# Optimization experiments

Measured on AMD Instinct MI355X. Metric: run time of the kernel, lower is better.

The kernel has to match this reference:

```python
import jax, jax.numpy as jnp
import numpy as np

BS, S, N, C, H, CP, T, CT, NB = 1, 2, 2048, 128, 8, 16, 512, 384, 3
DH = C // H
INF = 1.0e8

def _ln(x, w, b, eps=1e-5):
    mu = jnp.mean(x, axis=-1, keepdims=True)
    var = jnp.var(x, axis=-1, keepdims=True)
    return (x - mu) * jax.lax.rsqrt(var + eps) * w + b

def _ln_na(x, eps=1e-5):
    mu = jnp.mean(x, axis=-1, keepdims=True)
    var = jnp.var(x, axis=-1, keepdims=True)
    return (x - mu) * jax.lax.rsqrt(var + eps)

def _betas(n):
    # query row l belongs to window centered at 32*(l//32)+16; keys within +/- n_keys//2=64
    l = jnp.arange(n)
    centers = (l // 32) * 32 + 16
    m = jnp.arange(n)
    ok = (m[None, :] >= (centers - 64)[:, None]) & (m[None, :] < (centers + 64)[:, None])
    return jnp.where(ok, 0.0, -INF).astype(jnp.float32)

def setup_inputs():
    key = jax.random.key(0)
    ks = iter(jax.random.split(key, 80))
    def W(*shape):
        return jax.random.normal(next(ks), shape, dtype=jnp.float32) * 0.05
    return {
        "atom_single": jax.random.normal(next(ks), (BS, S, N, C), dtype=jnp.float32),
        "atom_proj": jax.random.normal(next(ks), (BS, N, C), dtype=jnp.float32),
        "atom_pair": jax.random.normal(next(ks), (BS, N, N, CP), dtype=jnp.float32),
        "mask": jnp.ones((BS, N), jnp.float32),
        "tok_idx": jnp.sort(jax.random.randint(next(ks), (BS, N), 0, T), axis=-1),
        "aln_s_w": jnp.ones((NB, C), jnp.float32), "aln_s_b": jnp.zeros((NB, C), jnp.float32),
        "aln_gate_w": W(NB, C, C), "aln_gate_b": jnp.zeros((NB, C), jnp.float32),
        "aln_shift_w": W(NB, C, C),
        "q_w": W(NB, C, C), "q_b": jnp.zeros((NB, C), jnp.float32),
        "k_w": W(NB, C, C), "v_w": W(NB, C, C),
        "pair_ln_w": jnp.ones((NB, CP), jnp.float32), "pair_ln_b": jnp.zeros((NB, CP), jnp.float32),
        "pair_w": W(NB, CP, H),
        "gate_w": W(NB, C, C), "out_w": W(NB, C, C),
        "og_w": W(NB, C, C), "og_b": jnp.full((NB, C), -2.0, jnp.float32),
        "t_aln_s_w": jnp.ones((NB, C), jnp.float32), "t_aln_s_b": jnp.zeros((NB, C), jnp.float32),
        "t_aln_gate_w": W(NB, C, C), "t_aln_gate_b": jnp.zeros((NB, C), jnp.float32),
        "t_aln_shift_w": W(NB, C, C),
        "t_a_w": W(NB, C, 2 * C), "t_b_w": W(NB, C, 2 * C),
        "t_out_w": W(NB, 2 * C, C),
        "t_og_w": W(NB, C, C), "t_og_b": jnp.full((NB, C), -2.0, jnp.float32),
        "tok_w": W(C, CT),
    }

def _forward(atom_single, atom_proj, atom_pair, mask, tok_idx, aln_s_w, aln_s_b, aln_gate_w, aln_gate_b, aln_shift_w, q_w, q_b, k_w, v_w, pair_ln_w, pair_ln_b, pair_w, gate_w, out_w, og_w, og_b, t_aln_s_w, t_aln_s_b, t_aln_gate_w, t_aln_gate_b, t_aln_shift_w, t_a_w, t_b_w, t_out_w, t_og_w, t_og_b, tok_w):
    betas = _betas(N)[None, None, None]                        # [1,1,1,N,N]
    mask_bias = ((mask - 1.0) * INF)[:, None, None, None, :]   # [bs,1,1,1,N]
    s = atom_proj[:, None]                                     # [bs,1,N,C]
    a = atom_single                                            # [bs,S,N,C]
    for i in range(NB):
        # AttentionPairBias with AdaLN conditioning on s
        sn = _ln(s, aln_s_w[i], aln_s_b[i])
        a1 = jax.nn.sigmoid(sn @ aln_gate_w[i] + aln_gate_b[i]) * _ln_na(a) + sn @ aln_shift_w[i]
        q = (a1 @ q_w[i] + q_b[i]).reshape(BS, S, N, H, DH)
        k = (a1 @ k_w[i]).reshape(BS, S, N, H, DH)
        v = (a1 @ v_w[i]).reshape(BS, S, N, H, DH)
        zb = _ln(atom_pair, pair_ln_w[i], pair_ln_b[i]) @ pair_w[i]    # [bs,N,N,H]
        zb = jnp.transpose(zb, (0, 3, 1, 2))[:, None]                  # [bs,1,H,N,N]
        logits = jnp.einsum('bsqhd,bskhd->bshqk', q, k) / np.float32(np.sqrt(DH)) + zb + betas + mask_bias
        p = jax.nn.softmax(logits, axis=-1)
        o = jnp.einsum('bshqk,bskhd->bsqhd', p, v).reshape(BS, S, N, C)
        o = (jax.nn.sigmoid(a1 @ gate_w[i]) * o) @ out_w[i]
        a = a + jax.nn.sigmoid(sn @ og_w[i] + og_b[i]) * o
        # ConditionedTransitionBlock (SwiGLU with adaLN-Zero gating)
        sn2 = _ln(s, t_aln_s_w[i], t_aln_s_b[i])
        a2 = jax.nn.sigmoid(sn2 @ t_aln_gate_w[i] + t_aln_gate_b[i]) * _ln_na(a) + sn2 @ t_aln_shift_w[i]
        hidden = jax.nn.silu(a2 @ t_a_w[i]) * (a2 @ t_b_w[i])
        a = a + jax.nn.sigmoid(sn2 @ t_og_w[i] + t_og_b[i]) * (hidden @ t_out_w[i])
    # project to token dim, relu, scatter-mean atoms -> tokens
    q_tok = jax.nn.relu(a @ tok_w)                             # [bs,S,N,CT]
    oh = jax.nn.one_hot(tok_idx, T, dtype=q_tok.dtype)         # [bs,N,T]
    cnt = jnp.clip(jnp.sum(oh, axis=1), 1.0)                   # [bs,T]
    tok = jnp.einsum('bsnc,bnt->bstc', q_tok, oh) / cnt[:, None, :, None]
    return tok

def reference(atom_single, atom_proj, atom_pair, mask, tok_idx, aln_s_w, aln_s_b, aln_gate_w, aln_gate_b, aln_shift_w, q_w, q_b, k_w, v_w, pair_ln_w, pair_ln_b, pair_w, gate_w, out_w, og_w, og_b, t_aln_s_w, t_aln_s_b, t_aln_gate_w, t_aln_gate_b, t_aln_shift_w, t_a_w, t_b_w, t_out_w, t_og_w, t_og_b, tok_w):
    return _forward(atom_single, atom_proj, atom_pair, mask, tok_idx, aln_s_w, aln_s_b, aln_gate_w, aln_gate_b, aln_shift_w, q_w, q_b, k_w, v_w, pair_ln_w, pair_ln_b, pair_w, gate_w, out_w, og_w, og_b, t_aln_s_w, t_aln_s_b, t_aln_gate_w, t_aln_gate_b, t_aln_shift_w, t_a_w, t_b_w, t_out_w, t_og_w, t_og_b, tok_w)
```

## Files before the change

### kernel.cpp

```cpp
#include <hip/hip_runtime.h>
#include <math.h>

#define NATOM 2048
#define CD 128
#define SD 2
#define TT 512
#define CTD 384
#define NBI 3
#define MR 4096

typedef unsigned short ushortx;
typedef __attribute__((ext_vector_type(8))) short bf16x8;
typedef __attribute__((ext_vector_type(4))) float f32x4;
typedef __attribute__((ext_vector_type(4))) unsigned short us4;

__device__ __forceinline__ float sigm(float x){ return 1.0f/(1.0f+expf(-x)); }
__device__ __forceinline__ ushortx f2b(float f){
  union { float f; unsigned u; } v; v.f = f;
  unsigned r = v.u + 0x7fffu + ((v.u>>16)&1u);
  return (ushortx)(r>>16);
}
__device__ __forceinline__ float b2f(ushortx u){
  union { unsigned u; float f; } v; v.u = ((unsigned)u)<<16; return v.f;
}
union U8 { ushortx u[8]; float4 v; };

#define OFFB_W3T    0ll
#define OFFB_B3     589824ll
#define OFFB_WQKVGT 599040ll
#define OFFB_BQ     992256ll
#define OFFB_WOUTT  998400ll
#define OFFB_WABT   1096704ll
#define OFFB_WTOUTT 1489920ll
#define OFFB_WTOKT  1686528ll
#define OFFB_SNP    2833408ll
#define OFFB_A      12270592ll
#define OFFB_QKVG   14367744ll
#define OFFB_ZB     18562048ll
#define OFFB_QTOK   31144960ll
#define OFFB_QKVG2  37436416ll

struct WPtrs {
  const float *aln_gate_w, *aln_gate_b, *aln_shift_w, *og_w, *og_b;
  const float *t_aln_gate_w, *t_aln_gate_b, *t_aln_shift_w, *t_og_w, *t_og_b;
  const float *q_w, *q_b, *k_w, *v_w, *gate_w, *out_w;
  const float *t_a_w, *t_b_w, *t_out_w, *tok_w;
};

__global__ __launch_bounds__(256) void prologue_kernel(WPtrs P, char* __restrict__ wsb,
  const float* __restrict__ atom_pair,
  const float* __restrict__ plw, const float* __restrict__ plb, const float* __restrict__ pw)
{
  int b = blockIdx.x;
  if (b < 3471){
    long long idx = (long long)b*256 + threadIdx.x;
    const long long s0=294912, s1=2304, s2=196608, s3=1536, s4=49152, s5=196608, s6=98304;
    if (idx < s0) {
      int which = (int)(idx/49152); int r = (int)(idx%49152); int n=r/128, k=r%128;
      int i = which>>1, t = which&1;
      const float* src;
      if (n<128)      src = (t?P.t_aln_gate_w :P.aln_gate_w ) + i*16384 + k*128 + n;
      else if (n<256) src = (t?P.t_aln_shift_w:P.aln_shift_w) + i*16384 + k*128 + (n-128);
      else            src = (t?P.t_og_w       :P.og_w       ) + i*16384 + k*128 + (n-256);
      ((ushortx*)(wsb+OFFB_W3T))[idx] = f2b(*src); return;
    }
    idx -= s0;
    if (idx < s1) {
      int which = (int)(idx/384); int col = (int)(idx%384); int i=which>>1, t=which&1;
      float v = 0.f;
      if (col<128)       v = (t?P.t_aln_gate_b:P.aln_gate_b)[i*128+col];
      else if (col>=256) v = (t?P.t_og_b      :P.og_b      )[i*128+col-256];
      ((float*)(wsb+OFFB_B3))[idx] = v; return;
    }
    idx -= s1;
    if (idx < s2) {
      int i = (int)(idx/65536); int r = (int)(idx%65536); int n=r/128, k=r%128;
      int seg = n>>7, c = n&127;
      const float* src = (seg==0?P.q_w: seg==1?P.k_w: seg==2?P.v_w: P.gate_w) + i*16384 + k*128 + c;
      ((ushortx*)(wsb+OFFB_WQKVGT))[idx] = f2b(*src); return;
    }
    idx -= s2;
    if (idx < s3) {
      int i = (int)(idx/512); int col = (int)(idx%512);
      ((float*)(wsb+OFFB_BQ))[idx] = (col<128) ? P.q_b[i*128+col] : 0.f; return;
    }
    idx -= s3;
    if (idx < s4) {
      int i = (int)(idx/16384); int r = (int)(idx%16384); int n=r/128, k=r%128;
      ((ushortx*)(wsb+OFFB_WOUTT))[idx] = f2b(P.out_w[i*16384 + k*128 + n]); return;
    }
    idx -= s4;
    if (idx < s5) {
      int i = (int)(idx/65536); int r = (int)(idx%65536); int n=r/128, k=r%128;
      const float* src = (n<256) ? P.t_a_w + i*32768 + k*256 + n
                                 : P.t_b_w + i*32768 + k*256 + (n-256);
      ((ushortx*)(wsb+OFFB_WABT))[idx] = f2b(*src); return;
    }
    idx -= s5;
    if (idx < s6) {
      int i = (int)(idx/32768); int r = (int)(idx%32768); int n=r/256, k=r%256;
      ((ushortx*)(wsb+OFFB_WTOUTT))[idx] = f2b(P.t_out_w[i*32768 + k*128 + n]); return;
    }
    idx -= s6;
    {
      int n = (int)(idx/128); int k = (int)(idx%128);
      ((ushortx*)(wsb+OFFB_WTOKT))[idx] = f2b(P.tok_w[k*384 + n]); return;
    }
  }
  {
    int idx = (b-3471)*256 + threadIdx.x;
    int q = idx>>7, j = idx&127;
    int m = (q & ~31) - 48 + j;
    bool ok = (m>=0 && m<NATOM);
    float x[16]; float mu=0.f, rs=0.f;
    if (ok){
      float s=0.f, sq=0.f;
      const float* p = atom_pair + ((long long)q*NATOM + m)*16;
      #pragma unroll
      for (int c=0;c<16;c++){ x[c]=p[c]; s+=x[c]; sq+=x[c]*x[c]; }
      mu = s*(1.f/16.f); float var = sq*(1.f/16.f)-mu*mu; rs = rsqrtf(var+1e-5f);
    }
    ushortx* zb = (ushortx*)(wsb+OFFB_ZB);
    #pragma unroll
    for (int it=0; it<NBI; it++){
      float out[8] = {0,0,0,0,0,0,0,0};
      if (ok){
        #pragma unroll
        for (int c=0;c<16;c++){
          float xn = (x[c]-mu)*rs*plw[it*16+c] + plb[it*16+c];
          #pragma unroll
          for (int h=0;h<8;h++) out[h] += xn * pw[it*128 + c*8 + h];
        }
      }
      #pragma unroll
      for (int h=0;h<8;h++)
        zb[(((long long)it*8+h)*NATOM + q)*128 + j] = f2b(out[h]);
    }
  }
}

template<int LAST>
__global__ __launch_bounds__(256) void fused_iter(
  const float* __restrict__ Afsrc,
  float* __restrict__ Af,
  const ushortx* __restrict__ QKVGin,
  const ushortx* __restrict__ zb,
  const float* __restrict__ mask,
  const ushortx* __restrict__ Wout,
  const ushortx* __restrict__ Wab,
  const ushortx* __restrict__ Wtout,
  const ushortx* __restrict__ WN,
  const float*   __restrict__ biasN,
  const ushortx* __restrict__ snpA,
  const ushortx* __restrict__ snpT,
  const ushortx* __restrict__ snpN,
  ushortx* __restrict__ QKVGout,
  float*   __restrict__ QTOK)
{
  __shared__ __align__(16) ushortx Bt[2][64][136];
  __shared__ __align__(16) float   Afr[16][132];
  __shared__ __align__(16) ushortx A2t[16][136];
  __shared__ __align__(16) ushortx Ht[16][264];
  __shared__ __align__(16) ushortx XX[16*264];
  __shared__ __align__(16) ushortx Kh[2][128][24];
  __shared__ __align__(16) ushortx Vh[2][128][24];
  __shared__ __align__(16) ushortx Zh[2][16][136];
  __shared__ __align__(16) ushortx Qh[2][16][16];
  __shared__ __align__(16) ushortx Gh[2][16][16];
  __shared__ __align__(16) float   Ls[16][132];
  __shared__ __align__(16) ushortx SnpT[16][392];
  __shared__ __align__(16) ushortx SnpN[16][392];
  __shared__ __align__(16) ushortx SnpAog[16][136];
  __shared__ float maskb[128];
  ushortx (*A1t)[136] = (ushortx(*)[136])XX;
  ushortx (*Hs)[264]  = (ushortx(*)[264])XX;

  int tid = threadIdx.x, rowBase = blockIdx.x*16;
  int sIdx = rowBase >> 11;
  int n0 = rowBase & 2047;
  int wbase = (n0 & ~31) - 48;
  int wave=tid>>6, lane=tid&63, lr=lane&15, lk=(lane>>4)*8;
  int wc = wave*16;
  int r = tid>>4, tcol = tid&15, c8 = tcol*8;
  long long grow = rowBase + r;
  int sr=tid>>2, csB=(tid&3)*32;
  int crow = (lane>>4)*4;

  { const float4* ap=(const float4*)&Afsrc[grow*128+c8];
    *(float4*)&Afr[r][c8]=ap[0]; *(float4*)&Afr[r][c8+4]=ap[1]; }
  if (tid < 128){
    int m = wbase + tid;
    maskb[tid] = (m>=0 && m<NATOM) ? (mask[m]-1.0f)*1e8f : -1e30f;
  }
  #pragma unroll
  for (int k=0;k<3;k++){ int idx=tid+k*256; int rr=idx/48, cc=(idx%48)*8;
    *(float4*)&SnpT[rr][cc] = *(const float4*)&snpT[(long long)((rowBase+rr)&2047)*384 + cc]; }
  if (!LAST){
    #pragma unroll
    for (int k=0;k<3;k++){ int idx=tid+k*256; int rr=idx/48, cc=(idx%48)*8;
      *(float4*)&SnpN[rr][cc] = *(const float4*)&snpN[(long long)((rowBase+rr)&2047)*384 + cc]; }
  }
  *(float4*)&SnpAog[r][c8] = *(const float4*)&snpA[(long long)((rowBase+r)&2047)*384 + 256 + c8];
  {
    const float4* bg = (const float4*)(Wout + (long long)sr*128 + csB);
    #pragma unroll
    for (int u=0;u<4;u++) *(float4*)&Bt[0][sr][csB+u*8] = bg[u];
  }

  int jr=tid>>1, hf=tid&1;
  int mm=wbase+jr; int mc = mm<0?0:(mm>NATOM-1?NATOM-1:mm);
  long long krow = ((long long)(sIdx*NATOM+mc))*512;
  auto issue = [&](int h, float4&kreg, float4&vreg, float4&zreg, float4&qg){
    kreg = *(const float4*)&QKVGin[krow + 128 + h*16 + hf*8];
    vreg = *(const float4*)&QKVGin[krow + 256 + h*16 + hf*8];
    zreg = *(const float4*)&zb[((long long)h*NATOM + n0 + r)*128 + c8];
    if (tid < 32)
      qg = *(const float4*)&QKVGin[((long long)(rowBase+(tid>>1)))*512 + h*16 + (tid&1)*8];
    else if (tid < 64){
      int tt=tid-32;
      qg = *(const float4*)&QKVGin[((long long)(rowBase+(tt>>1)))*512 + 384 + h*16 + (tt&1)*8];
    }
  };
  auto commit = [&](int bb, float4 kreg, float4 vreg, float4 zreg, float4 qg){
    *(float4*)&Kh[bb][jr][hf*8] = kreg;
    *(float4*)&Vh[bb][jr][hf*8] = vreg;
    *(float4*)&Zh[bb][r][c8] = zreg;
    if (tid < 32) *(float4*)&Qh[bb][tid>>1][(tid&1)*8] = qg;
    else if (tid < 64){ int tt=tid-32; *(float4*)&Gh[bb][tt>>1][(tt&1)*8] = qg; }
  };
  { float4 k0,v0,z0,q0 = make_float4(0,0,0,0);
    issue(0,k0,v0,z0,q0); commit(0,k0,v0,z0,q0); }
  __syncthreads();
  for (int h=0; h<8; ++h){
    int bb=h&1;
    float4 kn,vn,zn,qn = make_float4(0,0,0,0);
    if (h<7) issue(h+1,kn,vn,zn,qn);
    float qv[16];
    { U8 qa,qb_;
      qa.v=*(const float4*)&Qh[bb][r][0]; qb_.v=*(const float4*)&Qh[bb][r][8];
      #pragma unroll
      for (int t=0;t<8;t++){ qv[t]=b2f(qa.u[t]); qv[8+t]=b2f(qb_.u[t]); } }
    float lv[8], pmax=-1e30f;
    #pragma unroll
    for (int u=0;u<8;u++){
      int j=tcol+u*16;
      U8 ka,kb_;
      ka.v=*(const float4*)&Kh[bb][j][0]; kb_.v=*(const float4*)&Kh[bb][j][8];
      float dot=0.f;
      #pragma unroll
      for (int t=0;t<8;t++) dot += qv[t]*b2f(ka.u[t]);
      #pragma unroll
      for (int t=0;t<8;t++) dot += qv[8+t]*b2f(kb_.u[t]);
      float L = dot*0.25f + b2f(Zh[bb][r][j]) + maskb[j];
      lv[u]=L; pmax=fmaxf(pmax,L);
    }
    #pragma unroll
    for (int off=1; off<16; off<<=1) pmax = fmaxf(pmax, __shfl_xor(pmax,off));
    float ps=0.f;
    #pragma unroll
    for (int u=0;u<8;u++){ float e=expf(lv[u]-pmax); Ls[r][tcol+u*16]=e; ps+=e; }
    #pragma unroll
    for (int off=1; off<16; off<<=1) ps += __shfl_xor(ps,off);
    float inv = 1.0f/ps;
    __syncthreads();
    float a0=0.f;
    #pragma unroll 4
    for (int j=0;j<128;j++) a0 += Ls[r][j]*b2f(Vh[bb][j][tcol]);
    float gt = b2f(Gh[bb][r][tcol]);
    A1t[r][h*16+tcol] = f2b(sigm(gt)*a0*inv);
    if (h<7) commit((h+1)&1,kn,vn,zn,qn);
    __syncthreads();
  }

  const int NP = LAST ? 20 : 22;
  f32x4 acc = (f32x4){0.f,0.f,0.f,0.f};
  for (int p=0; p<NP; p++){
    __syncthreads();
    if (p+1 < NP){
      int pn = p+1;
      const ushortx* bsrc; long long bstride;
      if (pn<2)      { bsrc = Wout  + (long long)(pn*64)*128;                      bstride=128; }
      else if (pn<10){ bsrc = Wab   + (long long)((pn-2)*64)*128;                  bstride=128; }
      else if (pn<14){ int q=pn-10; bsrc = Wtout + (long long)((q>>1)*64)*256 + (q&1)*128; bstride=256; }
      else           { int q=pn-14; bsrc = WN    + (long long)(q*64)*128;          bstride=128; }
      const float4* bg=(const float4*)(bsrc + (long long)sr*bstride + csB);
      #pragma unroll
      for (int u=0;u<4;u++) *(float4*)&Bt[pn&1][sr][csB+u*8] = bg[u];
    }
    if (p==2){
      float x[8], s=0.f, sq=0.f;
      #pragma unroll
      for (int u=0;u<8;u++){ x[u]=Afr[r][c8+u]; s+=x[u]; sq+=x[u]*x[u]; }
      #pragma unroll
      for (int off=1; off<16; off<<=1){ s+=__shfl_xor(s,off); sq+=__shfl_xor(sq,off); }
      float mu=s*(1.f/128.f), rs=rsqrtf(sq*(1.f/128.f)-mu*mu+1e-5f);
      U8 ga,ha,pk;
      ga.v=*(const float4*)&SnpT[r][c8]; ha.v=*(const float4*)&SnpT[r][128+c8];
      #pragma unroll
      for (int t=0;t<8;t++) pk.u[t]=f2b(sigm(b2f(ga.u[t]))*((x[t]-mu)*rs)+b2f(ha.u[t]));
      *(float4*)&A2t[r][c8]=pk.v;
      __syncthreads();
    }
    if (p==14){
      float x[8], s=0.f, sq=0.f;
      #pragma unroll
      for (int u=0;u<8;u++){ x[u]=Afr[r][c8+u]; s+=x[u]; sq+=x[u]*x[u]; }
      { float4* ap=(float4*)&Af[grow*128+c8];
        ap[0]=*(float4*)&Afr[r][c8]; ap[1]=*(float4*)&Afr[r][c8+4]; }
      if (LAST){
        U8 pk;
        #pragma unroll
        for (int t=0;t<8;t++) pk.u[t]=f2b(x[t]);
        *(float4*)&A2t[r][c8]=pk.v;
      } else {
        #pragma unroll
        for (int off=1; off<16; off<<=1){ s+=__shfl_xor(s,off); sq+=__shfl_xor(sq,off); }
        float mu=s*(1.f/128.f), rs=rsqrtf(sq*(1.f/128.f)-mu*mu+1e-5f);
        U8 ga,ha,pk;
        ga.v=*(const float4*)&SnpN[r][c8]; ha.v=*(const float4*)&SnpN[r][128+c8];
        #pragma unroll
        for (int t=0;t<8;t++) pk.u[t]=f2b(sigm(b2f(ga.u[t]))*((x[t]-mu)*rs)+b2f(ha.u[t]));
        *(float4*)&A2t[r][c8]=pk.v;
      }
      __syncthreads();
    }
    if (p!=11 && p!=13) acc=(f32x4){0.f,0.f,0.f,0.f};
    #pragma unroll
    for (int ks=0; ks<4; ks++){
      bf16x8 a;
      if (p<2)       a = *(const bf16x8*)&A1t[lr][ks*32+lk];
      else if (p<10) a = *(const bf16x8*)&A2t[lr][ks*32+lk];
      else if (p<14){ int kc=(p-10)&1; a = *(const bf16x8*)&Hs[lr][kc*128+ks*32+lk]; }
      else           a = *(const bf16x8*)&A2t[lr][ks*32+lk];
      bf16x8 b = *(const bf16x8*)&Bt[p&1][wc+lr][ks*32+lk];
      acc = __builtin_amdgcn_mfma_f32_16x16x32_bf16(a,b,acc,0,0,0);
    }
    if (p<2){
      int ccol = p*64 + wc + lr;
      #pragma unroll
      for (int rr=0;rr<4;rr++){
        int rrow=crow+rr;
        float g=b2f(SnpAog[rrow][ccol]);
        Afr[rrow][ccol]+=sigm(g)*acc[rr];
      }
    } else if (p<10){
      int cp=p-2; int ccol=cp*64+wc+lr;
      if (cp<4){
        #pragma unroll
        for (int rr=0;rr<4;rr++) Ht[crow+rr][ccol]=f2b(acc[rr]);
      } else {
        int hc=ccol-256;
        #pragma unroll
        for (int rr=0;rr<4;rr++){
          float ha=b2f(Ht[crow+rr][hc]);
          Hs[crow+rr][hc]=f2b(ha*sigm(ha)*acc[rr]);
        }
      }
    } else if (p==11 || p==13){
      int cp=(p-10)>>1; int ccol=cp*64+wc+lr;
      #pragma unroll
      for (int rr=0;rr<4;rr++){
        int rrow=crow+rr;
        float g=b2f(SnpT[rrow][256+ccol]);
        Afr[rrow][ccol]+=sigm(g)*acc[rr];
      }
    } else if (p>=14){
      int q=p-14; int ccol=q*64+wc+lr;
      if (LAST){
        #pragma unroll
        for (int rr=0;rr<4;rr++)
          QTOK[(long long)(rowBase+crow+rr)*384 + ccol]=fmaxf(acc[rr],0.f);
      } else {
        float bv=biasN[ccol];
        #pragma unroll
        for (int rr=0;rr<4;rr++)
          QKVGout[(long long)(rowBase+crow+rr)*512 + ccol]=f2b(acc[rr]+bv);
      }
    }
  }
}

template<int AM, int BM>
__global__ __launch_bounds__(256) void gemm_f(
    const void* __restrict__ Asrc, long long strideA,
    const ushortx* __restrict__ B, long long strideB,
    const float* __restrict__ bias, long long strideBias,
    void* Cv, long long strideC,
    int M, int N, int K, int mode,
    const void* __restrict__ p1, const void* __restrict__ p2,
    const void* __restrict__ p3, const void* __restrict__ p4)
{
  constexpr int CG  = 256/BM;
  constexpr int XC  = 128/CG;
  constexpr int F4  = XC/8;
  constexpr int ACI = BM/32;
  int z = blockIdx.z;
  B += z*strideB;
  if (bias) bias += z*strideBias;
  float* C = (float*)Cv + z*strideC;
  ushortx* Cu = (ushortx*)Cv + z*strideC;
  __shared__ __align__(16) ushortx At[BM][136];
  __shared__ __align__(16) ushortx Bt[64][136];
  int tid = threadIdx.x;
  int rowBase = blockIdx.y*BM, colBase = blockIdx.x*64;
  int wave = tid>>6, lane = tid&63;
  int wr = (wave>>1)*(BM/2), wc = (wave&1)*32;
  int lr = lane&15, lk = (lane>>4)*8;
  f32x4 acc[ACI][2];
  #pragma unroll
  for (int i=0;i<ACI;i++)
    #pragma unroll
    for (int j=0;j<2;j++) acc[i][j] = (f32x4){0.f,0.f,0.f,0.f};

  int sr = tid/CG, q = tid%CG, cs = q*XC;
  int row = rowBase + sr;
  int bsr = tid>>2, bq = tid&3, bcs = bq*32;

  for (int kc=0; kc<K; kc+=128){
    if (kc) __syncthreads();
    {
      const float* arow = (const float*)Asrc + (long long)row*128;
      float x[XC]; float s=0.f, sq=0.f;
      const float4* ar = (const float4*)(arow + cs);
      #pragma unroll
      for (int u=0;u<XC/4;u++){
        float4 t = ar[u];
        x[4*u]=t.x; x[4*u+1]=t.y; x[4*u+2]=t.z; x[4*u+3]=t.w;
        s += t.x+t.y+t.z+t.w;
        sq += t.x*t.x+t.y*t.y+t.z*t.z+t.w*t.w;
      }
      #pragma unroll
      for (int off=1; off<CG; off<<=1){ s += __shfl_xor(s,off); sq += __shfl_xor(sq,off); }
      float mu = s*(1.f/128.f), var = sq*(1.f/128.f)-mu*mu;
      float rs = rsqrtf(var + 1e-5f);
      if (AM==1){
        const ushortx* sp = (const ushortx*)p1 + (long long)(row & (NATOM-1))*384;
        const float4* gr = (const float4*)(sp + cs);
        const float4* hr = (const float4*)(sp + 128 + cs);
        #pragma unroll
        for (int u=0;u<F4;u++){
          U8 ga, ha, pk;
          ga.v = gr[u]; ha.v = hr[u];
          #pragma unroll
          for (int t=0;t<8;t++)
            pk.u[t] = f2b(sigm(b2f(ga.u[t]))*((x[8*u+t]-mu)*rs) + b2f(ha.u[t]));
          *(float4*)&At[sr][cs+u*8] = pk.v;
        }
      } else {
        int iw = z>>1, tw = z&1;
        const float* w = (const float*)(tw?p3:p1) + iw*128;
        const float* b = (const float*)(tw?p4:p2) + iw*128;
        const float4* wrp = (const float4*)(w + cs);
        const float4* brp = (const float4*)(b + cs);
        #pragma unroll
        for (int u=0;u<F4;u++){
          float4 wa = wrp[2*u], wb = wrp[2*u+1];
          float4 ba = brp[2*u], bb = brp[2*u+1];
          U8 pk;
          pk.u[0]=f2b((x[8*u  ]-mu)*rs*wa.x+ba.x);
          pk.u[1]=f2b((x[8*u+1]-mu)*rs*wa.y+ba.y);
          pk.u[2]=f2b((x[8*u+2]-mu)*rs*wa.z+ba.z);
          pk.u[3]=f2b((x[8*u+3]-mu)*rs*wa.w+ba.w);
          pk.u[4]=f2b((x[8*u+4]-mu)*rs*wb.x+bb.x);
          pk.u[5]=f2b((x[8*u+5]-mu)*rs*wb.y+bb.y);
          pk.u[6]=f2b((x[8*u+6]-mu)*rs*wb.z+bb.z);
          pk.u[7]=f2b((x[8*u+7]-mu)*rs*wb.w+bb.w);
          *(float4*)&At[sr][cs+u*8] = pk.v;
        }
      }
    }
    {
      const float4* bg = (const float4*)(B + (long long)(colBase+bsr)*K + kc + bcs);
      #pragma unroll
      for (int u=0;u<4;u++) *(float4*)&Bt[bsr][bcs+u*8] = bg[u];
    }
    __syncthreads();
    #pragma unroll
    for (int ks=0; ks<4; ks++){
      bf16x8 b0 = *(const bf16x8*)&Bt[wc+lr][ks*32+lk];
      bf16x8 b1 = *(const bf16x8*)&Bt[wc+16+lr][ks*32+lk];
      #pragma unroll
      for (int i=0;i<ACI;i++){
        bf16x8 a = *(const bf16x8*)&At[wr+i*16+lr][ks*32+lk];
        acc[i][0] = __builtin_amdgcn_mfma_f32_16x16x32_bf16(a,b0,acc[i][0],0,0,0);
        acc[i][1] = __builtin_amdgcn_mfma_f32_16x16x32_bf16(a,b1,acc[i][1],0,0,0);
      }
    }
  }
  int crow0 = rowBase + wr + (lane>>4)*4;
  int ccol0 = colBase + wc + lr;
  #pragma unroll
  for (int i=0;i<ACI;i++){
    #pragma unroll
    for (int j=0;j<2;j++){
      int col = ccol0 + j*16;
      float bv = bias ? bias[col] : 0.f;
      #pragma unroll
      for (int rr=0; rr<4; rr++){
        int rrow = crow0 + i*16 + rr;
        float v = acc[i][j][rr] + bv;
        long long ci = (long long)rrow*N + col;
        Cu[ci] = f2b(v);
        (void)C; (void)mode;
      }
    }
  }
}

__global__ __launch_bounds__(128) void tokagg_kernel(const int* __restrict__ tok_idx,
    const float* __restrict__ qtok, float* __restrict__ out)
{
  int t = blockIdx.x;
  int lo=0, hi=NATOM;
  while (lo<hi){ int mid=(lo+hi)>>1; if (tok_idx[mid] < t) lo=mid+1; else hi=mid; }
  int start = lo;
  lo = start; hi = NATOM;
  while (lo<hi){ int mid=(lo+hi)>>1; if (tok_idx[mid] <= t) lo=mid+1; else hi=mid; }
  int end = lo;
  int cnt = end - start;
  float inv = 1.0f / (float)(cnt>0 ? cnt : 1);
  for (int s=0; s<SD; s++)
    for (int c=threadIdx.x; c<CTD; c+=128){
      float acc = 0.f;
      for (int n=start; n<end; n++) acc += qtok[((long long)(s*NATOM+n))*CTD + c];
      out[(long long)(s*TT + t)*CTD + c] = acc*inv;
    }
}

extern "C" void kernel_launch(void* const* d_in, const int* in_sizes, int n_in,
                              void* d_out, int out_size, void* d_ws, size_t ws_size,
                              hipStream_t stream)
{
  const float* atom_single = (const float*)d_in[0];
  const float* atom_proj   = (const float*)d_in[1];
  const float* atom_pair   = (const float*)d_in[2];
  const float* mask        = (const float*)d_in[3];
  const int*   tok_idx     = (const int*)  d_in[4];
  const float* aln_s_w     = (const float*)d_in[5];
  const float* aln_s_b     = (const float*)d_in[6];
  const float* pair_ln_w   = (const float*)d_in[14];
  const float* pair_ln_b   = (const float*)d_in[15];
  const float* pair_w      = (const float*)d_in[16];
  const float* t_aln_s_w   = (const float*)d_in[21];
  const float* t_aln_s_b   = (const float*)d_in[22];

  char* wsb = (char*)d_ws;
  ushortx* W3T    = (ushortx*)(wsb+OFFB_W3T);
  float*   B3     = (float*)  (wsb+OFFB_B3);
  ushortx* WQKVGT = (ushortx*)(wsb+OFFB_WQKVGT);
  float*   BQ     = (float*)  (wsb+OFFB_BQ);
  ushortx* WOUTT  = (ushortx*)(wsb+OFFB_WOUTT);
  ushortx* WABT   = (ushortx*)(wsb+OFFB_WABT);
  ushortx* WTOUTT = (ushortx*)(wsb+OFFB_WTOUTT);
  ushortx* WTOKT  = (ushortx*)(wsb+OFFB_WTOKT);
  ushortx* SNP    = (ushortx*)(wsb+OFFB_SNP);
  float*   Af     = (float*)  (wsb+OFFB_A);
  ushortx* QKVG   = (ushortx*)(wsb+OFFB_QKVG);
  ushortx* QKVG2  = (ushortx*)(wsb+OFFB_QKVG2);
  ushortx* ZB     = (ushortx*)(wsb+OFFB_ZB);
  float*   QTOK   = (float*)  (wsb+OFFB_QTOK);

  WPtrs P;
  P.aln_gate_w=(const float*)d_in[7];  P.aln_gate_b=(const float*)d_in[8];  P.aln_shift_w=(const float*)d_in[9];
  P.og_w=(const float*)d_in[19]; P.og_b=(const float*)d_in[20];
  P.t_aln_gate_w=(const float*)d_in[23]; P.t_aln_gate_b=(const float*)d_in[24]; P.t_aln_shift_w=(const float*)d_in[25];
  P.t_og_w=(const float*)d_in[29]; P.t_og_b=(const float*)d_in[30];
  P.q_w=(const float*)d_in[10]; P.q_b=(const float*)d_in[11]; P.k_w=(const float*)d_in[12];
  P.v_w=(const float*)d_in[13]; P.gate_w=(const float*)d_in[17]; P.out_w=(const float*)d_in[18];
  P.t_a_w=(const float*)d_in[26]; P.t_b_w=(const float*)d_in[27]; P.t_out_w=(const float*)d_in[28];
  P.tok_w=(const float*)d_in[31];

  prologue_kernel<<<4495,256,0,stream>>>(P, wsb, atom_pair,
      pair_ln_w, pair_ln_b, pair_w);
  gemm_f<4,64><<<dim3(6,32,6),256,0,stream>>>(atom_proj, 0, W3T, 49152ll,
      B3, 384ll, SNP, 786432ll, NATOM, 384, 128, 3,
      aln_s_w, aln_s_b, t_aln_s_w, t_aln_s_b);
  gemm_f<1,64><<<dim3(8,64,1),256,0,stream>>>(atom_single, 0, WQKVGT, 0,
      BQ, 0, QKVG, 0, MR, 512, 128, 3,
      SNP, nullptr, nullptr, nullptr);

  for (int i=0;i<NBI;i++){
    const ushortx* snpA = SNP + (long long)(2*i)*786432;
    const ushortx* snpT = SNP + (long long)(2*i+1)*786432;
    ushortx* qin  = (i&1) ? QKVG2 : QKVG;
    ushortx* qout = (i&1) ? QKVG  : QKVG2;
    const float* afsrc = (i==0) ? atom_single : Af;
    if (i < NBI-1){
      fused_iter<0><<<256,256,0,stream>>>(afsrc, Af, qin,
          ZB + (long long)i*2097152, mask,
          WOUTT + (long long)i*16384, WABT + (long long)i*65536, WTOUTT + (long long)i*32768,
          WQKVGT + (long long)(i+1)*65536, BQ + (long long)(i+1)*512,
          snpA, snpT, SNP + (long long)(2*(i+1))*786432,
          qout, nullptr);
    } else {
      fused_iter<1><<<256,256,0,stream>>>(afsrc, Af, qin,
          ZB + (long long)i*2097152, mask,
          WOUTT + (long long)i*16384, WABT + (long long)i*65536, WTOUTT + (long long)i*32768,
          WTOKT, nullptr,
          snpA, snpT, nullptr,
          qout, QTOK);
    }
  }
  tokagg_kernel<<<TT,128,0,stream>>>(tok_idx, QTOK, (float*)d_out);
}
```

Before: 579.6 us.

## Stage all-head K/V in LDS and fuse token scatter-mean into last iteration

The attention phase now loads the full K and V window (all heads, with an XOR swizzle on K) plus the pair bias into shared memory with one sync, instead of double-buffering each head over eight sync rounds. Heads are processed four at a time with staged probabilities. The separate token-aggregation kernel is removed: the last iteration atomically adds ReLU outputs pre-scaled by per-token inverse counts into an output zeroed in the prologue. Several small shared-memory staging buffers now read directly from global memory to fit the larger LDS footprint. The cost is higher LDS use, which may lower occupancy, plus atomic contention and a non-deterministic summation order.

```diff
diff --git a/kernel.cpp b/kernel.cpp
--- a/kernel.cpp
+++ b/kernel.cpp
@@ -33,11 +33,11 @@
 #define OFFB_WABT   1096704ll
 #define OFFB_WTOUTT 1489920ll
 #define OFFB_WTOKT  1686528ll
+#define OFFB_CNTI   1784832ll
 #define OFFB_SNP    2833408ll
 #define OFFB_A      12270592ll
 #define OFFB_QKVG   14367744ll
 #define OFFB_ZB     18562048ll
-#define OFFB_QTOK   31144960ll
 #define OFFB_QKVG2  37436416ll
 
 struct WPtrs {
@@ -49,7 +49,8 @@
 
 __global__ __launch_bounds__(256) void prologue_kernel(WPtrs P, char* __restrict__ wsb,
   const float* __restrict__ atom_pair,
-  const float* __restrict__ plw, const float* __restrict__ plb, const float* __restrict__ pw)
+  const float* __restrict__ plw, const float* __restrict__ plb, const float* __restrict__ pw,
+  const int* __restrict__ tok_idx, float* __restrict__ outbuf, int out_n)
 {
   int b = blockIdx.x;
   if (b < 3471){
@@ -107,7 +108,7 @@
       ((ushortx*)(wsb+OFFB_WTOKT))[idx] = f2b(P.tok_w[k*384 + n]); return;
     }
   }
-  {
+  if (b < 4495){
     int idx = (b-3471)*256 + threadIdx.x;
     int q = idx>>7, j = idx&127;
     int m = (q & ~31) - 48 + j;
@@ -136,15 +137,30 @@
       for (int h=0;h<8;h++)
         zb[(((long long)it*8+h)*NATOM + q)*128 + j] = f2b(out[h]);
     }
+    return;
+  }
+  if (b < 6031){
+    int i = (b-4495)*256 + threadIdx.x;
+    if (i < out_n) outbuf[i] = 0.f;
+    return;
+  }
+  {
+    float* CNTI = (float*)(wsb+OFFB_CNTI);
+    for (int t=threadIdx.x; t<TT; t+=256){
+      int lo=0, hi=NATOM;
+      while (lo<hi){ int mid=(lo+hi)>>1; if (tok_idx[mid] < t) lo=mid+1; else hi=mid; }
+      int st = lo; lo = st; hi = NATOM;
+      while (lo<hi){ int mid=(lo+hi)>>1; if (tok_idx[mid] <= t) lo=mid+1; else hi=mid; }
+      int cnt = lo - st;
+      CNTI[t] = 1.0f/(float)(cnt>0?cnt:1);
+    }
   }
 }
 
 template<int LAST>
 __global__ __launch_bounds__(256) void fused_iter(
-  const float* __restrict__ Afsrc,
-  float* __restrict__ Af,
-  const ushortx* __restrict__ QKVGin,
-  const ushortx* __restrict__ zb,
+  const float* __restrict__ Afsrc, float* __restrict__ Af,
+  const ushortx* __restrict__ QKVGin, const ushortx* __restrict__ zbg,
   const float* __restrict__ mask,
   const ushortx* __restrict__ Wout,
   const ushortx* __restrict__ Wab,
@@ -155,29 +171,31 @@
   const ushortx* __restrict__ snpT,
   const ushortx* __restrict__ snpN,
   ushortx* __restrict__ QKVGout,
-  float*   __restrict__ QTOK)
+  const int* __restrict__ tokidx, const float* __restrict__ CNTI,
+  float* __restrict__ OUT)
 {
-  __shared__ __align__(16) ushortx Bt[2][64][136];
-  __shared__ __align__(16) float   Afr[16][132];
-  __shared__ __align__(16) ushortx A2t[16][136];
-  __shared__ __align__(16) ushortx Ht[16][264];
+  __shared__ __align__(16) ushortx KST[128][128];
+  __shared__ __align__(16) ushortx VST[128][128];
+  __shared__ __align__(16) ushortx QST[16][128];
+  __shared__ __align__(16) char R1Raw[34816];
+  __shared__ __align__(16) char PRaw[33792];
+  __shared__ __align__(16) float Afr[16][132];
   __shared__ __align__(16) ushortx XX[16*264];
-  __shared__ __align__(16) ushortx Kh[2][128][24];
-  __shared__ __align__(16) ushortx Vh[2][128][24];
-  __shared__ __align__(16) ushortx Zh[2][16][136];
-  __shared__ __align__(16) ushortx Qh[2][16][16];
-  __shared__ __align__(16) ushortx Gh[2][16][16];
-  __shared__ __align__(16) float   Ls[16][132];
-  __shared__ __align__(16) ushortx SnpT[16][392];
-  __shared__ __align__(16) ushortx SnpN[16][392];
-  __shared__ __align__(16) ushortx SnpAog[16][136];
   __shared__ float maskb[128];
-  ushortx (*A1t)[136] = (ushortx(*)[136])XX;
-  ushortx (*Hs)[264]  = (ushortx(*)[264])XX;
+  __shared__ float invL[16][8];
+  __shared__ int   tokL[16];
+  __shared__ float invT[16];
+
+  ushortx (*Bt)[64][136]     = (ushortx(*)[64][136])R1Raw;
+  ushortx (*ZR)[16][4][128]  = (ushortx(*)[16][4][128])R1Raw;
+  float   (*Pm)[4][132]      = (float(*)[4][132])PRaw;
+  ushortx (*A2t)[136]        = (ushortx(*)[136])PRaw;
+  ushortx (*Ht)[264]         = (ushortx(*)[264])(PRaw + 4608);
+  ushortx (*A1t)[136]        = (ushortx(*)[136])XX;
+  ushortx (*Hs)[264]         = (ushortx(*)[264])XX;
 
   int tid = threadIdx.x, rowBase = blockIdx.x*16;
-  int sIdx = rowBase >> 11;
-  int n0 = rowBase & 2047;
+  int sIdx = rowBase>>11, n0 = rowBase&2047;
   int wbase = (n0 & ~31) - 48;
   int wave=tid>>6, lane=tid&63, lr=lane&15, lk=(lane>>4)*8;
   int wc = wave*16;
@@ -192,84 +210,108 @@
     int m = wbase + tid;
     maskb[tid] = (m>=0 && m<NATOM) ? (mask[m]-1.0f)*1e8f : -1e30f;
   }
+  if (LAST && tid < 16){
+    int t = tokidx[n0+tid]; tokL[tid]=t; invT[tid]=CNTI[t];
+  }
+  *(float4*)&QST[r][c8] = *(const float4*)&QKVGin[grow*512 + c8];
   #pragma unroll
-  for (int k=0;k<3;k++){ int idx=tid+k*256; int rr=idx/48, cc=(idx%48)*8;
-    *(float4*)&SnpT[rr][cc] = *(const float4*)&snpT[(long long)((rowBase+rr)&2047)*384 + cc]; }
-  if (!LAST){
+  for (int it=0; it<16; ++it){
+    int idx = tid + it*256;
+    int j = idx>>5, c = idx&31;
+    int m = wbase + j; int mc = m<0?0:(m>NATOM-1?NATOM-1:m);
+    long long rowb = ((long long)(sIdx*NATOM+mc))*512;
+    if (c < 16){
+      float4 v = *(const float4*)&QKVGin[rowb + 128 + c*8];
+      *(float4*)&KST[j][((c ^ (j>>3)) & 15)*8] = v;
+    } else {
+      int cv = c-16;
+      float4 v = *(const float4*)&QKVGin[rowb + 256 + cv*8];
+      *(float4*)&VST[j][cv*8] = v;
+    }
+  }
+  #pragma unroll
+  for (int it=0; it<8; ++it){
+    int idx = tid + it*256;
+    int hr = idx>>4, c = idx&15;
+    int h = hr>>4, rr = hr&15;
+    float4 v = *(const float4*)&zbg[((long long)h*NATOM + n0 + rr)*128 + c*8];
+    *(float4*)&ZR[h>>2][rr][h&3][c*8] = v;
+  }
+  __syncthreads();
+
+  #pragma unroll
+  for (int half=0; half<2; ++half){
     #pragma unroll
-    for (int k=0;k<3;k++){ int idx=tid+k*256; int rr=idx/48, cc=(idx%48)*8;
-      *(float4*)&SnpN[rr][cc] = *(const float4*)&snpN[(long long)((rowBase+rr)&2047)*384 + cc]; }
-  }
-  *(float4*)&SnpAog[r][c8] = *(const float4*)&snpA[(long long)((rowBase+r)&2047)*384 + 256 + c8];
+    for (int hl=0; hl<4; ++hl){
+      int h = half*4 + hl;
+      float qv[16];
+      { U8 qa, qb_;
+        qa.v = *(const float4*)&QST[r][h*16];
+        qb_.v = *(const float4*)&QST[r][h*16+8];
+        #pragma unroll
+        for (int t=0;t<8;t++){ qv[t]=b2f(qa.u[t]); qv[8+t]=b2f(qb_.u[t]); } }
+      U8 za; za.v = *(const float4*)&ZR[half][r][hl][c8];
+      int cs0 = (2*h) ^ tcol;
+      int cs1 = (2*h+1) ^ tcol;
+      float lv[8], pmax=-1e30f;
+      #pragma unroll
+      for (int u=0;u<8;u++){
+        int j = c8 + u;
+        U8 ka, kb_;
+        ka.v = *(const float4*)&KST[j][cs0*8];
+        kb_.v = *(const float4*)&KST[j][cs1*8];
+        float dot = 0.f;
+        #pragma unroll
+        for (int t=0;t<8;t++) dot += qv[t]*b2f(ka.u[t]);
+        #pragma unroll
+        for (int t=0;t<8;t++) dot += qv[8+t]*b2f(kb_.u[t]);
+        float L = dot*0.25f + b2f(za.u[u]) + maskb[j];
+        lv[u]=L; pmax=fmaxf(pmax,L);
+      }
+      #pragma unroll
+      for (int off=1; off<16; off<<=1) pmax = fmaxf(pmax, __shfl_xor(pmax,off));
+      float4 e0, e1;
+      e0.x=expf(lv[0]-pmax); e0.y=expf(lv[1]-pmax); e0.z=expf(lv[2]-pmax); e0.w=expf(lv[3]-pmax);
+      e1.x=expf(lv[4]-pmax); e1.y=expf(lv[5]-pmax); e1.z=expf(lv[6]-pmax); e1.w=expf(lv[7]-pmax);
+      float ps = e0.x+e0.y+e0.z+e0.w+e1.x+e1.y+e1.z+e1.w;
+      *(float4*)&Pm[r][hl][c8]   = e0;
+      *(float4*)&Pm[r][hl][c8+4] = e1;
+      #pragma unroll
+      for (int off=1; off<16; off<<=1) ps += __shfl_xor(ps,off);
+      if (tcol == hl) invL[r][h] = 1.0f/ps;
+    }
+    __syncthreads();
+    {
+      int hh = tcol>>2, d0 = half*64 + tcol*4;
+      float a0=0.f,a1=0.f,a2=0.f,a3=0.f;
+      const float* prow = &Pm[r][hh][0];
+      #pragma unroll 8
+      for (int j4=0; j4<128; j4+=4){
+        float4 pj = *(const float4*)&prow[j4];
+        us4 v0 = *(const us4*)&VST[j4  ][d0];
+        us4 v1 = *(const us4*)&VST[j4+1][d0];
+        us4 v2 = *(const us4*)&VST[j4+2][d0];
+        us4 v3 = *(const us4*)&VST[j4+3][d0];
+        a0 += pj.x*b2f(v0[0]); a1 += pj.x*b2f(v0[1]); a2 += pj.x*b2f(v0[2]); a3 += pj.x*b2f(v0[3]);
+        a0 += pj.y*b2f(v1[0]); a1 += pj.y*b2f(v1[1]); a2 += pj.y*b2f(v1[2]); a3 += pj.y*b2f(v1[3]);
+        a0 += pj.z*b2f(v2[0]); a1 += pj.z*b2f(v2[1]); a2 += pj.z*b2f(v2[2]); a3 += pj.z*b2f(v2[3]);
+        a0 += pj.w*b2f(v3[0]); a1 += pj.w*b2f(v3[1]); a2 += pj.w*b2f(v3[2]); a3 += pj.w*b2f(v3[3]);
+      }
+      float inv = invL[r][half*4+hh];
+      us4 gt = *(const us4*)&QKVGin[grow*512 + 384 + d0];
+      us4 st;
+      st[0]=f2b(sigm(b2f(gt[0]))*a0*inv);
+      st[1]=f2b(sigm(b2f(gt[1]))*a1*inv);
+      st[2]=f2b(sigm(b2f(gt[2]))*a2*inv);
+      st[3]=f2b(sigm(b2f(gt[3]))*a3*inv);
+      *(us4*)&A1t[r][d0] = st;
+    }
+    if (half==0) __syncthreads();
+  }
   {
     const float4* bg = (const float4*)(Wout + (long long)sr*128 + csB);
     #pragma unroll
     for (int u=0;u<4;u++) *(float4*)&Bt[0][sr][csB+u*8] = bg[u];
-  }
-
-  int jr=tid>>1, hf=tid&1;
-  int mm=wbase+jr; int mc = mm<0?0:(mm>NATOM-1?NATOM-1:mm);
-  long long krow = ((long long)(sIdx*NATOM+mc))*512;
-  auto issue = [&](int h, float4&kreg, float4&vreg, float4&zreg, float4&qg){
-    kreg = *(const float4*)&QKVGin[krow + 128 + h*16 + hf*8];
-    vreg = *(const float4*)&QKVGin[krow + 256 + h*16 + hf*8];
-    zreg = *(const float4*)&zb[((long long)h*NATOM + n0 + r)*128 + c8];
-    if (tid < 32)
-      qg = *(const float4*)&QKVGin[((long long)(rowBase+(tid>>1)))*512 + h*16 + (tid&1)*8];
-    else if (tid < 64){
-      int tt=tid-32;
-      qg = *(const float4*)&QKVGin[((long long)(rowBase+(tt>>1)))*512 + 384 + h*16 + (tt&1)*8];
-    }
-  };
-  auto commit = [&](int bb, float4 kreg, float4 vreg, float4 zreg, float4 qg){
-    *(float4*)&Kh[bb][jr][hf*8] = kreg;
-    *(float4*)&Vh[bb][jr][hf*8] = vreg;
-    *(float4*)&Zh[bb][r][c8] = zreg;
-    if (tid < 32) *(float4*)&Qh[bb][tid>>1][(tid&1)*8] = qg;
-    else if (tid < 64){ int tt=tid-32; *(float4*)&Gh[bb][tt>>1][(tt&1)*8] = qg; }
-  };
-  { float4 k0,v0,z0,q0 = make_float4(0,0,0,0);
-    issue(0,k0,v0,z0,q0); commit(0,k0,v0,z0,q0); }
-  __syncthreads();
-  for (int h=0; h<8; ++h){
-    int bb=h&1;
-    float4 kn,vn,zn,qn = make_float4(0,0,0,0);
-    if (h<7) issue(h+1,kn,vn,zn,qn);
-    float qv[16];
-    { U8 qa,qb_;
-      qa.v=*(const float4*)&Qh[bb][r][0]; qb_.v=*(const float4*)&Qh[bb][r][8];
-      #pragma unroll
-      for (int t=0;t<8;t++){ qv[t]=b2f(qa.u[t]); qv[8+t]=b2f(qb_.u[t]); } }
-    float lv[8], pmax=-1e30f;
-    #pragma unroll
-    for (int u=0;u<8;u++){
-      int j=tcol+u*16;
-      U8 ka,kb_;
-      ka.v=*(const float4*)&Kh[bb][j][0]; kb_.v=*(const float4*)&Kh[bb][j][8];
-      float dot=0.f;
-      #pragma unroll
-      for (int t=0;t<8;t++) dot += qv[t]*b2f(ka.u[t]);
-      #pragma unroll
-      for (int t=0;t<8;t++) dot += qv[8+t]*b2f(kb_.u[t]);
-      float L = dot*0.25f + b2f(Zh[bb][r][j]) + maskb[j];
-      lv[u]=L; pmax=fmaxf(pmax,L);
-    }
-    #pragma unroll
-    for (int off=1; off<16; off<<=1) pmax = fmaxf(pmax, __shfl_xor(pmax,off));
-    float ps=0.f;
-    #pragma unroll
-    for (int u=0;u<8;u++){ float e=expf(lv[u]-pmax); Ls[r][tcol+u*16]=e; ps+=e; }
-    #pragma unroll
-    for (int off=1; off<16; off<<=1) ps += __shfl_xor(ps,off);
-    float inv = 1.0f/ps;
-    __syncthreads();
-    float a0=0.f;
-    #pragma unroll 4
-    for (int j=0;j<128;j++) a0 += Ls[r][j]*b2f(Vh[bb][j][tcol]);
-    float gt = b2f(Gh[bb][r][tcol]);
-    A1t[r][h*16+tcol] = f2b(sigm(gt)*a0*inv);
-    if (h<7) commit((h+1)&1,kn,vn,zn,qn);
-    __syncthreads();
   }
 
   const int NP = LAST ? 20 : 22;
@@ -294,8 +336,8 @@
       #pragma unroll
       for (int off=1; off<16; off<<=1){ s+=__shfl_xor(s,off); sq+=__shfl_xor(sq,off); }
       float mu=s*(1.f/128.f), rs=rsqrtf(sq*(1.f/128.f)-mu*mu+1e-5f);
-      U8 ga,ha,pk;
-      ga.v=*(const float4*)&SnpT[r][c8]; ha.v=*(const float4*)&SnpT[r][128+c8];
+      const ushortx* sp = snpT + (long long)((int)grow&2047)*384;
+      U8 ga,ha,pk; ga.v=*(const float4*)&sp[c8]; ha.v=*(const float4*)&sp[128+c8];
       #pragma unroll
       for (int t=0;t<8;t++) pk.u[t]=f2b(sigm(b2f(ga.u[t]))*((x[t]-mu)*rs)+b2f(ha.u[t]));
       *(float4*)&A2t[r][c8]=pk.v;
@@ -316,8 +358,8 @@
         #pragma unroll
         for (int off=1; off<16; off<<=1){ s+=__shfl_xor(s,off); sq+=__shfl_xor(sq,off); }
         float mu=s*(1.f/128.f), rs=rsqrtf(sq*(1.f/128.f)-mu*mu+1e-5f);
-        U8 ga,ha,pk;
-        ga.v=*(const float4*)&SnpN[r][c8]; ha.v=*(const float4*)&SnpN[r][128+c8];
+        const ushortx* sp = snpN + (long long)((int)grow&2047)*384;
+        U8 ga,ha,pk; ga.v=*(const float4*)&sp[c8]; ha.v=*(const float4*)&sp[128+c8];
         #pragma unroll
         for (int t=0;t<8;t++) pk.u[t]=f2b(sigm(b2f(ga.u[t]))*((x[t]-mu)*rs)+b2f(ha.u[t]));
         *(float4*)&A2t[r][c8]=pk.v;
@@ -340,7 +382,7 @@
       #pragma unroll
       for (int rr=0;rr<4;rr++){
         int rrow=crow+rr;
-        float g=b2f(SnpAog[rrow][ccol]);
+        float g=b2f(snpA[(long long)((rowBase+rrow)&2047)*384 + 256 + ccol]);
         Afr[rrow][ccol]+=sigm(g)*acc[rr];
       }
     } else if (p<10){
@@ -361,15 +403,20 @@
       #pragma unroll
       for (int rr=0;rr<4;rr++){
         int rrow=crow+rr;
-        float g=b2f(SnpT[rrow][256+ccol]);
+        float g=b2f(snpT[(long long)((rowBase+rrow)&2047)*384 + 256 + ccol]);
         Afr[rrow][ccol]+=sigm(g)*acc[rr];
       }
     } else if (p>=14){
       int q=p-14; int ccol=q*64+wc+lr;
       if (LAST){
         #pragma unroll
-        for (int rr=0;rr<4;rr++)
-          QTOK[(long long)(rowBase+crow+rr)*384 + ccol]=fmaxf(acc[rr],0.f);
+        for (int rr=0;rr<4;rr++){
+          int rloc = crow+rr;
+          int rowg = rowBase + rloc;
+          int s = rowg>>11;
+          float v = fmaxf(acc[rr],0.f) * invT[rloc];
+          atomicAdd(&OUT[((long long)(s*TT + tokL[rloc])*CTD) + ccol], v);
+        }
       } else {
         float bv=biasN[ccol];
         #pragma unroll
@@ -397,7 +444,6 @@
   int z = blockIdx.z;
   B += z*strideB;
   if (bias) bias += z*strideBias;
-  float* C = (float*)Cv + z*strideC;
   ushortx* Cu = (ushortx*)Cv + z*strideC;
   __shared__ __align__(16) ushortx At[BM][136];
   __shared__ __align__(16) ushortx Bt[64][136];
@@ -501,30 +547,10 @@
         float v = acc[i][j][rr] + bv;
         long long ci = (long long)rrow*N + col;
         Cu[ci] = f2b(v);
-        (void)C; (void)mode;
-      }
-    }
-  }
-}
-
-__global__ __launch_bounds__(128) void tokagg_kernel(const int* __restrict__ tok_idx,
-    const float* __restrict__ qtok, float* __restrict__ out)
-{
-  int t = blockIdx.x;
-  int lo=0, hi=NATOM;
-  while (lo<hi){ int mid=(lo+hi)>>1; if (tok_idx[mid] < t) lo=mid+1; else hi=mid; }
-  int start = lo;
-  lo = start; hi = NATOM;
-  while (lo<hi){ int mid=(lo+hi)>>1; if (tok_idx[mid] <= t) lo=mid+1; else hi=mid; }
-  int end = lo;
-  int cnt = end - start;
-  float inv = 1.0f / (float)(cnt>0 ? cnt : 1);
-  for (int s=0; s<SD; s++)
-    for (int c=threadIdx.x; c<CTD; c+=128){
-      float acc = 0.f;
-      for (int n=start; n<end; n++) acc += qtok[((long long)(s*NATOM+n))*CTD + c];
-      out[(long long)(s*TT + t)*CTD + c] = acc*inv;
-    }
+        (void)mode;
+      }
+    }
+  }
 }
 
 extern "C" void kernel_launch(void* const* d_in, const int* in_sizes, int n_in,
@@ -553,12 +579,12 @@
   ushortx* WABT   = (ushortx*)(wsb+OFFB_WABT);
   ushortx* WTOUTT = (ushortx*)(wsb+OFFB_WTOUTT);
   ushortx* WTOKT  = (ushortx*)(wsb+OFFB_WTOKT);
+  float*   CNTI   = (float*)  (wsb+OFFB_CNTI);
   ushortx* SNP    = (ushortx*)(wsb+OFFB_SNP);
   float*   Af     = (float*)  (wsb+OFFB_A);
   ushortx* QKVG   = (ushortx*)(wsb+OFFB_QKVG);
   ushortx* QKVG2  = (ushortx*)(wsb+OFFB_QKVG2);
   ushortx* ZB     = (ushortx*)(wsb+OFFB_ZB);
-  float*   QTOK   = (float*)  (wsb+OFFB_QTOK);
 
   WPtrs P;
   P.aln_gate_w=(const float*)d_in[7];  P.aln_gate_b=(const float*)d_in[8];  P.aln_shift_w=(const float*)d_in[9];
@@ -570,8 +596,8 @@
   P.t_a_w=(const float*)d_in[26]; P.t_b_w=(const float*)d_in[27]; P.t_out_w=(const float*)d_in[28];
   P.tok_w=(const float*)d_in[31];
 
-  prologue_kernel<<<4495,256,0,stream>>>(P, wsb, atom_pair,
-      pair_ln_w, pair_ln_b, pair_w);
+  prologue_kernel<<<6032,256,0,stream>>>(P, wsb, atom_pair,
+      pair_ln_w, pair_ln_b, pair_w, tok_idx, (float*)d_out, SD*TT*CTD);
   gemm_f<4,64><<<dim3(6,32,6),256,0,stream>>>(atom_proj, 0, W3T, 49152ll,
       B3, 384ll, SNP, 786432ll, NATOM, 384, 128, 3,
       aln_s_w, aln_s_b, t_aln_s_w, t_aln_s_b);
@@ -591,15 +617,14 @@
           WOUTT + (long long)i*16384, WABT + (long long)i*65536, WTOUTT + (long long)i*32768,
           WQKVGT + (long long)(i+1)*65536, BQ + (long long)(i+1)*512,
           snpA, snpT, SNP + (long long)(2*(i+1))*786432,
-          qout, nullptr);
+          qout, nullptr, nullptr, nullptr);
     } else {
       fused_iter<1><<<256,256,0,stream>>>(afsrc, Af, qin,
           ZB + (long long)i*2097152, mask,
           WOUTT + (long long)i*16384, WABT + (long long)i*65536, WTOUTT + (long long)i*32768,
           WTOKT, nullptr,
           snpA, snpT, nullptr,
-          qout, QTOK);
-    }
-  }
-  tokagg_kernel<<<TT,128,0,stream>>>(tok_idx, QTOK, (float*)d_out);
+          qout, tok_idx, CNTI, (float*)d_out);
+    }
+  }
 }
```

Result: faster. 557.0 us (-3.9%).
